# Kernel optimization log

Measured on AMD Instinct MI355X. Metric: run time of the kernel, lower is better.

## Reference

```python
import jax, jax.numpy as jnp
import numpy as np

B, S, D, H, HD, L, E, K, F = 1, 1024, 1024, 16, 64, 64, 8, 2, 4096
EPS = 1e-6


def rms_norm(x):
    return x / jnp.sqrt(jnp.mean(x * x, axis=-1, keepdims=True) + EPS)


def rope_sincos(seq, dim):
    # standard GPT-NeoX-style rotary tables, shape [seq, dim]
    inv = 1.0 / (10000.0 ** (jnp.arange(0, dim, 2, dtype=jnp.float32) / dim))
    ang = jnp.arange(seq, dtype=jnp.float32)[:, None] * inv[None, :]
    sin = jnp.concatenate([jnp.sin(ang), jnp.sin(ang)], axis=-1)
    cos = jnp.concatenate([jnp.cos(ang), jnp.cos(ang)], axis=-1)
    return sin, cos


def apply_rotary(x, sin, cos):
    d = x.shape[-1] // 2
    rot = jnp.concatenate([-x[..., d:], x[..., :d]], axis=-1)
    return x * cos + rot * sin


def setup_inputs() -> dict:
    key = jax.random.key(0)
    ks = jax.random.split(key, 16)
    sd = 0.02

    def nrm(k, shp):
        return jax.random.normal(k, shp, jnp.float32) * sd

    return dict(
        x=jax.random.normal(ks[0], (B, S, D), jnp.float32),
        noise_u=jax.random.uniform(ks[1], (B, S, E), jnp.float32),
        Wdkv=nrm(ks[2], (H, L, HD)),      # per-head w_dkv  (torch weight [L,HD])
        Wq=nrm(ks[3], (H, HD, HD)),       # per-head wq
        Wuv=nrm(ks[4], (H, L, HD)),       # per-head w_uv
        Wuk=nrm(ks[5], (H, L, HD)),       # per-head w_uk
        Wk_rope=nrm(ks[6], (H, L, HD)),   # per-head w_k_rope
        Wq_rope=nrm(ks[7], (H, HD, L)),   # per-head w_q_rope weight
        bq_rope=jnp.zeros((H, HD), jnp.float32),  # w_q_rope bias (Linear default bias=True)
        Wo_head=nrm(ks[8], (H, HD, HD)),  # per-head w_o (no bias)
        Wr=nrm(ks[9], (E, D)),            # router weight
        Wn=nrm(ks[10], (E, D)),           # noise weight
        r_bias=jnp.zeros((E,), jnp.float32),
        W1=nrm(ks[11], (E, D, F)),        # expert fc1 (transposed torch layout)
        b1=jnp.zeros((E, F), jnp.float32),
        W2=nrm(ks[12], (E, F, D)),        # expert fc2
        b2=jnp.zeros((E, D), jnp.float32),
    )


def reference(x, noise_u, Wdkv, Wq, Wuv, Wuk, Wk_rope, Wq_rope, bq_rope,
              Wo_head, Wr, Wn, r_bias, W1, b1, W2, b2):
    # ---- multi-head latent attention (vectorized over heads) ----
    y = rms_norm(x)
    xs = y.reshape(B, S, H, HD).transpose(0, 2, 1, 3)  # [B,H,S,HD]
    sin_k, cos_k = rope_sincos(S, L)
    sin_q, cos_q = rope_sincos(S, HD)

    k = apply_rotary(jnp.einsum('bhsd,hld->bhsl', xs, Wk_rope), sin_k, cos_k)  # [B,H,S,L]
    ckv = jnp.einsum('bhsd,hld->bhsl', xs, Wdkv)                               # [B,H,S,L]
    q = jnp.einsum('bhsl,hdl->bhsd', ckv, Wq_rope) + bq_rope[None, :, None, :]
    q = apply_rotary(q, sin_q, cos_q)                                          # [B,H,S,HD]

    absorbed = jnp.einsum('hqe,hle->hql', Wq, Wuk)                             # [H,HD,L]
    s1 = jnp.einsum('bhsd,hdl,bhtl->bhst', xs, absorbed, ckv)
    s2 = jnp.einsum('bhsd,bhtd->bhst', q, k)
    scores = (s1 + s2) / jnp.sqrt(jnp.float32(2 * HD))
    mask = jnp.tril(jnp.ones((S, S), dtype=bool))  # past_length = 0
    scores = jnp.where(mask, scores, -jnp.inf)
    attn = jax.nn.softmax(scores, axis=-1)

    v = jnp.einsum('bhsl,hld->bhsd', ckv, Wuv)
    o = jnp.einsum('bhst,bhtd->bhsd', attn, v)
    o = jnp.einsum('bhsd,hed->bhse', o, Wo_head)  # per-head w_o (no bias)
    attn_out = o.transpose(0, 2, 1, 3).reshape(B, S, D)
    x = x + attn_out

    # ---- noisy top-k MoE ----
    y2 = rms_norm(x)
    logits = jnp.einsum('bsd,ed->bse', y2, Wr)
    noisy = jnp.einsum('bsd,ed->bse', y2, Wn)
    nl = noise_u * jax.nn.softplus(noisy) + logits + r_bias
    topv, topi = jax.lax.top_k(nl, K)
    gates = jax.nn.softmax(topv, axis=-1)  # softmax over -inf-scattered logits == softmax over top-k
    probs = jnp.sum(gates[..., None] * jax.nn.one_hot(topi, E, dtype=x.dtype), axis=-2)  # [B,S,E]

    h = jax.nn.gelu(jnp.einsum('bsd,edf->ebsf', y2, W1) + b1[:, None, None, :], approximate=False)
    eo = jnp.einsum('ebsf,efd->ebsd', h, W2) + b2[:, None, None, :]
    moe_out = jnp.einsum('bse,ebsd->bsd', probs, eo)
    return x + moe_out
```

## Files before the change

kernel.cpp:

```cpp
#include <hip/hip_runtime.h>
#include <math.h>

#define S_ 1024
#define D_ 1024
#define H_ 16
#define F_ 4096

typedef short s16x8 __attribute__((ext_vector_type(8)));
typedef float fx4 __attribute__((ext_vector_type(4)));

__device__ __forceinline__ float bf2f(unsigned int u){
  union { float f; unsigned int u; } v; v.u = u<<16; return v.f;
}
__device__ __forceinline__ unsigned short f2bf(float f){
  union { float f; unsigned int u; } v; v.f = f;
  unsigned int r = v.u + 0x7fffu + ((v.u>>16)&1u);
  return (unsigned short)(r>>16);
}
__device__ __forceinline__ unsigned int pk2(float a, float b){
  return (unsigned int)f2bf(a) | ((unsigned int)f2bf(b)<<16);
}
__device__ __forceinline__ void gld16(const void* g, void* l){
  typedef const unsigned int __attribute__((address_space(1)))* gp_t;
  typedef unsigned int __attribute__((address_space(3)))* lp_t;
  __builtin_amdgcn_global_load_lds((gp_t)g, (lp_t)l, 16, 0, 0);
}
__device__ __forceinline__ int xcd_swz(int bid, int nwg){
  int q = nwg >> 3;
  return (bid & 7)*q + (bid >> 3);
}

__global__ __launch_bounds__(256) void k_rmsnorm(const float* __restrict__ x, unsigned short* __restrict__ y){
  int row = blockIdx.x, t = threadIdx.x;
  const float4 v = ((const float4*)(x + (size_t)row*D_))[t];
  float ss = v.x*v.x + v.y*v.y + v.z*v.z + v.w*v.w;
  #pragma unroll
  for(int o=1;o<64;o<<=1) ss += __shfl_xor(ss, o);
  __shared__ float red[4];
  if((t&63)==0) red[t>>6]=ss;
  __syncthreads();
  float sc = rsqrtf((red[0]+red[1]+red[2]+red[3])*(1.0f/D_) + 1e-6f);
  ushort4 o4;
  o4.x=f2bf(v.x*sc); o4.y=f2bf(v.y*sc); o4.z=f2bf(v.z*sc); o4.w=f2bf(v.w*sc);
  ((ushort4*)(y + (size_t)row*D_))[t]=o4;
}

__global__ __launch_bounds__(256) void k_prep(const float* __restrict__ Wq,
    const float* __restrict__ Wuk, const float* __restrict__ Wuv,
    float* __restrict__ abs_t, float* __restrict__ wuvt){
  int h = blockIdx.x, tid = threadIdx.x;
  __shared__ float wq[4096], wuk[4096];
  for(int i=tid;i<4096;i+=256){ wq[i]=Wq[h*4096+i]; wuk[i]=Wuk[h*4096+i]; }
  __syncthreads();
  for(int i=tid;i<4096;i+=256){
    float a=0.f;
    #pragma unroll 8
    for(int e=0;e<64;e++) a += wq[(i&63)*64+e]*wuk[(i>>6)*64+e];
    abs_t[h*4096+i]=a;
    wuvt[h*4096+i]=Wuv[h*4096 + (i&63)*64 + (i>>6)];
  }
}

__device__ __forceinline__ void stage_B64(const float* __restrict__ W, unsigned short* Bs, int tid){
  int n = tid>>2, kq = tid&3;
  const float* s = W + n*64 + kq*16;
  float4 f0=*(const float4*)(s), f1=*(const float4*)(s+4), f2=*(const float4*)(s+8), f3=*(const float4*)(s+12);
  ushort4 u0,u1,u2,u3;
  u0.x=f2bf(f0.x);u0.y=f2bf(f0.y);u0.z=f2bf(f0.z);u0.w=f2bf(f0.w);
  u1.x=f2bf(f1.x);u1.y=f2bf(f1.y);u1.z=f2bf(f1.z);u1.w=f2bf(f1.w);
  u2.x=f2bf(f2.x);u2.y=f2bf(f2.y);u2.z=f2bf(f2.z);u2.w=f2bf(f2.w);
  u3.x=f2bf(f3.x);u3.y=f2bf(f3.y);u3.z=f2bf(f3.z);u3.w=f2bf(f3.w);
  int sl0=((kq*2)^(n&7))*8, sl1=((kq*2+1)^(n&7))*8;
  *(ushort4*)&Bs[n*64+sl0]=u0;   *(ushort4*)&Bs[n*64+sl0+4]=u1;
  *(ushort4*)&Bs[n*64+sl1]=u2;   *(ushort4*)&Bs[n*64+sl1+4]=u3;
}
__device__ __forceinline__ void gemm64(const unsigned short* Asrc, const unsigned short* Bs,
    int wv, int l16, int l4, fx4 acc[4]){
  int srow = wv*16 + l16;
  #pragma unroll
  for(int kb=0;kb<2;kb++){
    s16x8 af = *(const s16x8*)&Asrc[srow*64 + (((kb*4+l4)^(srow&7))*8)];
    #pragma unroll
    for(int nf=0;nf<4;nf++){
      int n = nf*16+l16;
      s16x8 bf = *(const s16x8*)&Bs[n*64 + (((kb*4+l4)^(n&7))*8)];
      acc[nf] = __builtin_amdgcn_mfma_f32_16x16x32_bf16(af, bf, acc[nf], 0,0,0);
    }
  }
}

__global__ __launch_bounds__(256) void k_proj_m(const unsigned short* __restrict__ y,
    const float* __restrict__ abs_t, const float* __restrict__ wuvt,
    const float* __restrict__ Wdkv, const float* __restrict__ Wk_rope,
    const float* __restrict__ Wq_rope, const float* __restrict__ bq_rope,
    unsigned short* __restrict__ kk, unsigned short* __restrict__ qq,
    unsigned short* __restrict__ vv){
  __shared__ unsigned short ysd[4096];
  __shared__ unsigned short ckvs[4096];
  __shared__ unsigned short Bs[4096];
  __shared__ unsigned short tmp[64*72];
  const float LNC = 0.28782313662425575f;
  const float ASC = 0.08838834764831845f;
  int s0 = blockIdx.x*64, h = blockIdx.y, tid = threadIdx.x;
  int wv = tid>>6, lane = tid&63, l16 = lane&15, l4 = lane>>4;
  fx4 acc[4];

  {
    int rg = lane>>3, sg = (lane&7)^(rg&7);
    #pragma unroll
    for(int c2=0;c2<2;c2++){
      int c = wv*2+c2;
      gld16(y + (size_t)(s0+c*8+rg)*D_ + h*64 + sg*8, &ysd[c*512]);
    }
  }
  stage_B64(Wdkv + h*4096, Bs, tid);
  __syncthreads();

  #pragma unroll
  for(int nf=0;nf<4;nf++){acc[nf][0]=0.f;acc[nf][1]=0.f;acc[nf][2]=0.f;acc[nf][3]=0.f;}
  gemm64(ysd, Bs, wv, l16, l4, acc);
  #pragma unroll
  for(int nf=0;nf<4;nf++){
    int col = nf*16+l16;
    #pragma unroll
    for(int r=0;r<4;r++){
      int srow = wv*16+4*l4+r;
      ckvs[srow*64 + (((col>>3)^(srow&7))*8) + (col&7)] = f2bf(acc[nf][r]);
    }
  }
  __syncthreads();
  { int row=tid>>2, sl=(tid&3)*2;
    uint4 a=*(const uint4*)&ckvs[row*64+sl*8];
    uint4 b=*(const uint4*)&ckvs[row*64+sl*8+8];
    unsigned short* kr = kk + ((size_t)(h*S_)+s0+row)*128;
    *(uint4*)&kr[(sl^(row&7))*8]=a;
    *(uint4*)&kr[((sl+1)^(row&7))*8]=b;
  }
  stage_B64(Wk_rope + h*4096, Bs, tid);
  __syncthreads();

  #pragma unroll
  for(int nf=0;nf<4;nf++){acc[nf][0]=0.f;acc[nf][1]=0.f;acc[nf][2]=0.f;acc[nf][3]=0.f;}
  gemm64(ysd, Bs, wv, l16, l4, acc);
  #pragma unroll
  for(int nf=0;nf<2;nf++){
    int llo = nf*16+l16;
    float inv = __expf(-(float)llo * LNC);
    #pragma unroll
    for(int r=0;r<4;r++){
      int srow = wv*16+4*l4+r;
      float sn,cs; __sincosf((float)(s0+srow)*inv,&sn,&cs);
      float alo=acc[nf][r], ahi=acc[nf+2][r];
      tmp[srow*72 + llo]      = f2bf(alo*cs - ahi*sn);
      tmp[srow*72 + llo + 32] = f2bf(ahi*cs + alo*sn);
    }
  }
  __syncthreads();
  { int row=tid>>2, c=(tid&3)*16;
    uint4 a=*(const uint4*)&tmp[row*72+c]; uint4 b=*(const uint4*)&tmp[row*72+c+8];
    unsigned short* kr = kk + ((size_t)(h*S_)+s0+row)*128 + 64;
    *(uint4*)&kr[c]=a; *(uint4*)&kr[c+8]=b; }
  stage_B64(Wq_rope + h*4096, Bs, tid);
  __syncthreads();

  #pragma unroll
  for(int nf=0;nf<4;nf++){acc[nf][0]=0.f;acc[nf][1]=0.f;acc[nf][2]=0.f;acc[nf][3]=0.f;}
  gemm64(ckvs, Bs, wv, l16, l4, acc);
  #pragma unroll
  for(int nf=0;nf<4;nf++){
    float bq = bq_rope[h*64 + nf*16+l16];
    #pragma unroll
    for(int r=0;r<4;r++) acc[nf][r]+=bq;
  }
  #pragma unroll
  for(int nf=0;nf<2;nf++){
    int dlo = nf*16+l16;
    float inv = __expf(-(float)dlo * LNC);
    #pragma unroll
    for(int r=0;r<4;r++){
      int srow = wv*16+4*l4+r;
      float sn,cs; __sincosf((float)(s0+srow)*inv,&sn,&cs);
      float alo=acc[nf][r]*ASC, ahi=acc[nf+2][r]*ASC;
      tmp[srow*72 + dlo]      = f2bf(alo*cs - ahi*sn);
      tmp[srow*72 + dlo + 32] = f2bf(ahi*cs + alo*sn);
    }
  }
  __syncthreads();
  { int row=tid>>2, c=(tid&3)*16;
    uint4 a=*(const uint4*)&tmp[row*72+c]; uint4 b=*(const uint4*)&tmp[row*72+c+8];
    unsigned short* qr = qq + ((size_t)(h*S_)+s0+row)*128 + 64;
    *(uint4*)&qr[c]=a; *(uint4*)&qr[c+8]=b; }
  stage_B64(abs_t + h*4096, Bs, tid);
  __syncthreads();

  #pragma unroll
  for(int nf=0;nf<4;nf++){acc[nf][0]=0.f;acc[nf][1]=0.f;acc[nf][2]=0.f;acc[nf][3]=0.f;}
  gemm64(ysd, Bs, wv, l16, l4, acc);
  #pragma unroll
  for(int nf=0;nf<4;nf++)
    #pragma unroll
    for(int r=0;r<4;r++)
      tmp[(wv*16+4*l4+r)*72 + nf*16+l16] = f2bf(acc[nf][r]*ASC);
  __syncthreads();
  { int row=tid>>2, c=(tid&3)*16;
    uint4 a=*(const uint4*)&tmp[row*72+c]; uint4 b=*(const uint4*)&tmp[row*72+c+8];
    unsigned short* qr = qq + ((size_t)(h*S_)+s0+row)*128;
    *(uint4*)&qr[c]=a; *(uint4*)&qr[c+8]=b; }
  stage_B64(wuvt + h*4096, Bs, tid);
  __syncthreads();

  #pragma unroll
  for(int nf=0;nf<4;nf++){acc[nf][0]=0.f;acc[nf][1]=0.f;acc[nf][2]=0.f;acc[nf][3]=0.f;}
  gemm64(ckvs, Bs, wv, l16, l4, acc);
  #pragma unroll
  for(int nf=0;nf<4;nf++)
    #pragma unroll
    for(int r=0;r<4;r++)
      tmp[(wv*16+4*l4+r)*72 + nf*16+l16] = f2bf(acc[nf][r]);
  __syncthreads();
  { int row=tid>>2, c=(tid&3)*16;
    uint4 a=*(const uint4*)&tmp[row*72+c]; uint4 b=*(const uint4*)&tmp[row*72+c+8];
    unsigned short* vr = vv + ((size_t)(h*S_)+s0+row)*64;
    *(uint4*)&vr[c]=a; *(uint4*)&vr[c+8]=b; }
}

__global__ __launch_bounds__(256) void k_attn2(const unsigned short* __restrict__ qq,
    const unsigned short* __restrict__ kk, const unsigned short* __restrict__ vv,
    const float* __restrict__ Wo, const float* __restrict__ x, float* __restrict__ x1){
  __shared__ unsigned short Ks[64*128];
  __shared__ unsigned short Vt[64*72];
  __shared__ unsigned short Pl[4][16*72];
  int h = blockIdx.y, q0 = blockIdx.x*64, tid = threadIdx.x;
  int wave = tid>>6, lane = tid&63;
  int l16 = lane&15, l4 = lane>>4;
  int qglob = q0 + wave*16 + l16;

  s16x8 qf[4];
  {
    const unsigned short* qp = qq + ((size_t)(h*S_)+qglob)*128 + l4*8;
    #pragma unroll
    for(int kb=0;kb<4;kb++) qf[kb] = *(const s16x8*)(qp + kb*32);
  }
  fx4 ot[4];
  #pragma unroll
  for(int t=0;t<4;t++){ ot[t][0]=0.f; ot[t][1]=0.f; ot[t][2]=0.f; ot[t][3]=0.f; }
  float mrun=-1e30f, lrun=0.f;
  int nkt = blockIdx.x + 1;

  for(int kt=0;kt<nkt;kt++){
    int kt0 = kt*64;
    __syncthreads();
    #pragma unroll
    for(int it=0;it<4;it++){
      int idx = tid + it*256;
      int row = idx>>4, c = idx&15;
      uint4 u = *(const uint4*)(kk + ((size_t)(h*S_)+kt0+row)*128 + c*8);
      *(uint4*)&Ks[row*128 + ((c^(row&7))<<3)] = u;
    }
    #pragma unroll
    for(int it=0;it<2;it++){
      int idx = tid + it*256;
      int k = idx>>3, d0 = (idx&7)*8;
      uint4 u = *(const uint4*)(vv + ((size_t)(h*S_)+kt0+k)*64 + d0);
      unsigned short t8[8];
      *(uint4*)t8 = u;
      #pragma unroll
      for(int j=0;j<8;j++) Vt[(d0+j)*72 + k] = t8[j];
    }
    __syncthreads();

    fx4 sa[4];
    #pragma unroll
    for(int i=0;i<4;i++){ sa[i][0]=0.f; sa[i][1]=0.f; sa[i][2]=0.f; sa[i][3]=0.f; }
    #pragma unroll
    for(int kb=0;kb<4;kb++){
      #pragma unroll
      for(int i=0;i<4;i++){
        int row = 16*i + l16;
        s16x8 ak = *(const s16x8*)&Ks[row*128 + (((l4+4*kb)^(row&7))<<3)];
        sa[i] = __builtin_amdgcn_mfma_f32_16x16x32_bf16(ak, qf[kb], sa[i], 0,0,0);
      }
    }
    float pv[16]; float mloc=-1e30f;
    #pragma unroll
    for(int i=0;i<4;i++)
      #pragma unroll
      for(int r=0;r<4;r++){
        int kg = kt0 + 16*i + 4*l4 + r;
        float s = (kg<=qglob)? sa[i][r] : -1e30f;
        pv[i*4+r]=s; mloc=fmaxf(mloc,s);
      }
    mloc = fmaxf(mloc, __shfl_xor(mloc,16));
    mloc = fmaxf(mloc, __shfl_xor(mloc,32));
    float mnew = fmaxf(mrun,mloc);
    float alpha = __expf(mrun-mnew);
    float psum=0.f;
    #pragma unroll
    for(int z=0;z<16;z++){ pv[z]=__expf(pv[z]-mnew); psum+=pv[z]; }
    psum += __shfl_xor(psum,16); psum += __shfl_xor(psum,32);
    lrun = lrun*alpha + psum; mrun = mnew;
    #pragma unroll
    for(int t=0;t<4;t++){ ot[t][0]*=alpha; ot[t][1]*=alpha; ot[t][2]*=alpha; ot[t][3]*=alpha; }
    {
      unsigned short* pw = &Pl[wave][l16*72 + 4*l4];
      #pragma unroll
      for(int i=0;i<4;i++){
        *(unsigned int*)&pw[16*i]   = pk2(pv[i*4+0],pv[i*4+1]);
        *(unsigned int*)&pw[16*i+2] = pk2(pv[i*4+2],pv[i*4+3]);
      }
    }
    #pragma unroll
    for(int kb=0;kb<2;kb++){
      s16x8 pf = *(const s16x8*)&Pl[wave][l16*72 + kb*32 + l4*8];
      #pragma unroll
      for(int t=0;t<4;t++){
        s16x8 av = *(const s16x8*)&Vt[(16*t+l16)*72 + kb*32 + l4*8];
        ot[t] = __builtin_amdgcn_mfma_f32_16x16x32_bf16(av, pf, ot[t], 0,0,0);
      }
    }
  }

  float invl = 1.f/lrun;
  {
    unsigned short* pw = &Pl[wave][l16*72 + 4*l4];
    #pragma unroll
    for(int t=0;t<4;t++){
      *(unsigned int*)&pw[16*t]   = pk2(ot[t][0]*invl, ot[t][1]*invl);
      *(unsigned int*)&pw[16*t+2] = pk2(ot[t][2]*invl, ot[t][3]*invl);
    }
  }
  __syncthreads();
  #pragma unroll
  for(int it=0;it<4;it++){
    int idx = tid + it*256;
    int ee = idx>>4, dd = (idx&15)*4;
    float4 wv = *(const float4*)(Wo + h*4096 + ee*64 + dd);
    ushort4 w4; w4.x=f2bf(wv.x); w4.y=f2bf(wv.y); w4.z=f2bf(wv.z); w4.w=f2bf(wv.w);
    *(ushort4*)&Vt[ee*72 + dd] = w4;
  }
  __syncthreads();
  fx4 outT[4];
  #pragma unroll
  for(int t=0;t<4;t++){ outT[t][0]=0.f; outT[t][1]=0.f; outT[t][2]=0.f; outT[t][3]=0.f; }
  #pragma unroll
  for(int kb=0;kb<2;kb++){
    s16x8 of = *(const s16x8*)&Pl[wave][l16*72 + kb*32 + l4*8];
    #pragma unroll
    for(int t=0;t<4;t++){
      s16x8 aw = *(const s16x8*)&Vt[(16*t+l16)*72 + kb*32 + l4*8];
      outT[t] = __builtin_amdgcn_mfma_f32_16x16x32_bf16(aw, of, outT[t], 0,0,0);
    }
  }
  #pragma unroll
  for(int t=0;t<4;t++){
    size_t base = (size_t)qglob*D_ + h*64 + 16*t + 4*l4;
    float4 xv = *(const float4*)(x + base);
    float4 r;
    r.x = xv.x + outT[t][0]; r.y = xv.y + outT[t][1];
    r.z = xv.z + outT[t][2]; r.w = xv.w + outT[t][3];
    *(float4*)(x1+base) = r;
  }
}

__global__ __launch_bounds__(64) void k_gate(const float* __restrict__ x1, const float* __restrict__ Wr,
    const float* __restrict__ Wn, const float* __restrict__ r_bias, const float* __restrict__ noise_u,
    float* __restrict__ gates, int* __restrict__ topi, unsigned short* __restrict__ y2){
  int s = blockIdx.x, lane = threadIdx.x;
  const float* xr = x1 + (size_t)s*D_ + lane*16;
  float yv[16]; float ss=0.f;
  #pragma unroll
  for(int i=0;i<16;i+=4){
    float4 a = *(const float4*)(xr+i);
    yv[i]=a.x; yv[i+1]=a.y; yv[i+2]=a.z; yv[i+3]=a.w;
    ss += a.x*a.x+a.y*a.y+a.z*a.z+a.w*a.w;
  }
  #pragma unroll
  for(int o=1;o<64;o<<=1) ss += __shfl_xor(ss,o);
  float sc = rsqrtf(ss*(1.0f/D_) + 1e-6f);
  #pragma unroll
  for(int i=0;i<16;i++) yv[i]*=sc;
  {
    unsigned short* yo = y2 + (size_t)s*D_ + lane*16;
    ushort4 o0,o1,o2,o3;
    o0.x=f2bf(yv[0]); o0.y=f2bf(yv[1]); o0.z=f2bf(yv[2]); o0.w=f2bf(yv[3]);
    o1.x=f2bf(yv[4]); o1.y=f2bf(yv[5]); o1.z=f2bf(yv[6]); o1.w=f2bf(yv[7]);
    o2.x=f2bf(yv[8]); o2.y=f2bf(yv[9]); o2.z=f2bf(yv[10]); o2.w=f2bf(yv[11]);
    o3.x=f2bf(yv[12]); o3.y=f2bf(yv[13]); o3.z=f2bf(yv[14]); o3.w=f2bf(yv[15]);
    *(ushort4*)(yo)   = o0; *(ushort4*)(yo+4) = o1;
    *(ushort4*)(yo+8) = o2; *(ushort4*)(yo+12)= o3;
  }
  float lg[8], nz[8];
  #pragma unroll
  for(int e=0;e<8;e++){
    const float* wr = Wr + e*D_ + lane*16;
    const float* wn = Wn + e*D_ + lane*16;
    float a=0.f,b=0.f;
    #pragma unroll
    for(int i=0;i<16;i+=4){
      float4 w1 = *(const float4*)(wr+i); float4 w2 = *(const float4*)(wn+i);
      a += yv[i]*w1.x + yv[i+1]*w1.y + yv[i+2]*w1.z + yv[i+3]*w1.w;
      b += yv[i]*w2.x + yv[i+1]*w2.y + yv[i+2]*w2.z + yv[i+3]*w2.w;
    }
    lg[e]=a; nz[e]=b;
  }
  #pragma unroll
  for(int o=1;o<64;o<<=1){
    #pragma unroll
    for(int e=0;e<8;e++){ lg[e]+=__shfl_xor(lg[e],o); nz[e]+=__shfl_xor(nz[e],o); }
  }
  if(lane==0){
    float nl[8];
    for(int e=0;e<8;e++){
      float z = nz[e];
      float sp = (z>20.f)? z : log1pf(expf(z));
      nl[e] = noise_u[s*8+e]*sp + lg[e] + r_bias[e];
    }
    int i0=0; float v0=nl[0];
    for(int e=1;e<8;e++) if(nl[e]>v0){v0=nl[e];i0=e;}
    float v1=-1e30f; int i1=0;
    for(int e=0;e<8;e++) if(e!=i0 && nl[e]>v1){v1=nl[e];i1=e;}
    float ex = expf(v1-v0);
    gates[s*2]   = 1.f/(1.f+ex);
    gates[s*2+1] = ex/(1.f+ex);
    topi[s*2]=i0; topi[s*2+1]=i1;
  }
}

__global__ __launch_bounds__(256) void k_lists(const int* __restrict__ topi,
    int* __restrict__ offs, int* __restrict__ pair_tok, int* __restrict__ slot_of){
  __shared__ int tp[2048];
  __shared__ int cnt[8];
  __shared__ int off_s[9];
  int t = threadIdx.x;
  int wave = t>>6, lane = t&63;
  unsigned long long below = (lane==63)? 0xFFFFFFFFFFFFFFFFull>>1
                                       : ((1ull<<lane)-1ull);
  for(int i=t;i<2048;i+=256) tp[i]=topi[i];
  __syncthreads();
  #pragma unroll
  for(int sub=0;sub<2;sub++){
    int e = wave*2+sub;
    int c=0;
    for(int ch=0;ch<32;ch++) c += (tp[ch*64+lane]==e);
    #pragma unroll
    for(int o=1;o<64;o<<=1) c += __shfl_xor(c,o);
    if(lane==0) cnt[e]=c;
  }
  __syncthreads();
  if(t==0){
    int a=0;
    for(int e=0;e<8;e++){ off_s[e]=a; a += (cnt[e]+127)&~127; }
    off_s[8]=a;
    for(int e=0;e<9;e++) offs[e]=off_s[e];
  }
  __syncthreads();
  #pragma unroll
  for(int sub=0;sub<2;sub++){
    int e = wave*2+sub;
    int base = off_s[e];
    for(int ch=0;ch<32;ch++){
      int idx = ch*64+lane;
      bool pred = (tp[idx]==e);
      unsigned long long mask = __ballot(pred);
      if(pred){
        int slot = base + __popcll(mask & below);
        pair_tok[slot] = idx>>1;
        slot_of[idx] = slot;
      }
      base += __popcll(mask);
    }
    for(int slot=base+lane; slot<off_s[e+1]; slot+=64) pair_tok[slot]=0;
  }
}

__global__ __launch_bounds__(256) void k_cvt_t(const float* __restrict__ src,
    unsigned short* __restrict__ dst, int R, int C){
  __shared__ float ts[64][65];
  int e = blockIdx.z;
  int r0 = blockIdx.x*64, c0 = blockIdx.y*64;
  const float* s = src + (size_t)e*R*C;
  unsigned short* d = dst + (size_t)e*R*C;
  int t = threadIdx.x;
  #pragma unroll
  for(int it=0; it<4; it++){
    int flat = it*256+t;
    int r = flat>>4, cq = (flat&15)*4;
    float4 v = *(const float4*)(s + (size_t)(r0+r)*C + c0+cq);
    ts[r][cq]=v.x; ts[r][cq+1]=v.y; ts[r][cq+2]=v.z; ts[r][cq+3]=v.w;
  }
  __syncthreads();
  #pragma unroll
  for(int it=0; it<4; it++){
    int flat = it*256+t;
    int c = flat>>4, kq = (flat&15)*4;
    ushort4 o;
    o.x=f2bf(ts[kq][c]); o.y=f2bf(ts[kq+1][c]); o.z=f2bf(ts[kq+2][c]); o.w=f2bf(ts[kq+3][c]);
    *(ushort4*)(d + (size_t)(c0+c)*R + r0+kq) = o;
  }
}

__global__ __launch_bounds__(256) void k_fc1t(const unsigned short* __restrict__ y2,
    const int* __restrict__ pair_tok, const int* __restrict__ offs,
    const unsigned short* __restrict__ Bt, const float* __restrict__ bias1,
    unsigned short* __restrict__ hbuf){
  __shared__ unsigned short As[2][8192];
  __shared__ unsigned short Bs[2][8192];
  __shared__ int sh_e;
  int tid=threadIdx.x, lane=tid&63, wv=tid>>6;
  int swz = xcd_swz(blockIdx.x, 768);
  int r0 = (swz % 24)*128, n0 = (swz / 24)*128;
  if(tid==0){ int e=-1; if(r0<offs[8]){e=0; while(offs[e+1]<=r0) e++;} sh_e=e; }
  __syncthreads();
  int e=sh_e; if(e<0) return;
  int rg = lane>>3;
  int sg = (lane&7)^(rg&7);
  const unsigned short* aptr[4];
  const unsigned short* bptr[4];
  #pragma unroll
  for(int c=0;c<4;c++){
    int ch = wv*4+c;
    int tok = pair_tok[r0 + ch*8 + rg];
    aptr[c] = y2 + (size_t)tok*D_ + sg*8;
    bptr[c] = Bt + (size_t)e*D_*F_ + (size_t)(n0 + ch*8 + rg)*D_ + sg*8;
  }
  int l16=lane&15, l4=lane>>4;
  int wm=wv>>1, wn=wv&1;
  fx4 acc[4][4];
  #pragma unroll
  for(int a0=0;a0<4;a0++)
    #pragma unroll
    for(int b0=0;b0<4;b0++){ acc[a0][b0][0]=0.f; acc[a0][b0][1]=0.f; acc[a0][b0][2]=0.f; acc[a0][b0][3]=0.f; }

  #pragma unroll
  for(int c=0;c<4;c++){
    gld16(aptr[c], &As[0][(wv*4+c)*512]);
    gld16(bptr[c], &Bs[0][(wv*4+c)*512]);
  }

  int buf=0;
  for(int kt=0;kt<D_;kt+=64){
    asm volatile("s_waitcnt vmcnt(0)" ::: "memory");
    asm volatile("s_barrier" ::: "memory");
    s16x8 af[2][4], bf[2][4];
    #pragma unroll
    for(int kb=0;kb<2;kb++){
      #pragma unroll
      for(int mf=0;mf<4;mf++){
        int row = wm*64+mf*16+l16;
        af[kb][mf] = *(const s16x8*)&As[buf][row*64 + (((kb*4+l4)^(row&7))*8)];
      }
      #pragma unroll
      for(int nf=0;nf<4;nf++){
        int col = wn*64+nf*16+l16;
        bf[kb][nf] = *(const s16x8*)&Bs[buf][col*64 + (((kb*4+l4)^(col&7))*8)];
      }
    }
    if(kt+64<D_){
      #pragma unroll
      for(int c=0;c<4;c++){
        gld16(aptr[c]+kt+64, &As[buf^1][(wv*4+c)*512]);
        gld16(bptr[c]+kt+64, &Bs[buf^1][(wv*4+c)*512]);
      }
    }
    __builtin_amdgcn_sched_barrier(0);
    __builtin_amdgcn_s_setprio(1);
    #pragma unroll
    for(int kb=0;kb<2;kb++)
      #pragma unroll
      for(int mf=0;mf<4;mf++)
        #pragma unroll
        for(int nf=0;nf<4;nf++)
          acc[mf][nf]=__builtin_amdgcn_mfma_f32_16x16x32_bf16(af[kb][mf],bf[kb][nf],acc[mf][nf],0,0,0);
    __builtin_amdgcn_s_setprio(0);
    asm volatile("s_barrier" ::: "memory");
    buf ^= 1;
  }
  #pragma unroll
  for(int mf=0;mf<4;mf++)
    #pragma unroll
    for(int nf=0;nf<4;nf++){
      int gcol=n0+wn*64+nf*16+l16;
      float bias=bias1[e*F_+gcol];
      #pragma unroll
      for(int rgi=0;rgi<4;rgi++){
        int grow=r0+wm*64+mf*16+l4*4+rgi;
        float vv=acc[mf][nf][rgi]+bias;
        float g=0.5f*vv*(1.f+erff(vv*0.70710678118654752f));
        hbuf[(size_t)grow*F_+gcol]=f2bf(g);
      }
    }
}

__global__ __launch_bounds__(256) void k_fc2t(const unsigned short* __restrict__ hbuf,
    const int* __restrict__ offs, const unsigned short* __restrict__ Bt,
    const float* __restrict__ bias2, float* __restrict__ eo, int klen, int parts){
  __shared__ unsigned short As[2][8192];
  __shared__ unsigned short Bs[2][4096];
  __shared__ int sh_e;
  int tid=threadIdx.x, lane=tid&63, wv=tid>>6;
  int nwg = 384*parts;
  int swz = xcd_swz(blockIdx.x, nwg);
  int kz  = swz / 384;
  int rem = swz % 384;
  int r0 = (rem % 24)*128, n0 = (rem / 24)*64;
  int k0 = kz*klen;
  if(tid==0){ int e=-1; if(r0<offs[8]){e=0; while(offs[e+1]<=r0) e++;} sh_e=e; }
  __syncthreads();
  int e=sh_e; if(e<0) return;
  int rg = lane>>3;
  int sg = (lane&7)^(rg&7);
  const unsigned short* aptr[4];
  const unsigned short* bptr[2];
  #pragma unroll
  for(int c=0;c<4;c++){
    int ch = wv*4+c;
    aptr[c] = hbuf + (size_t)(r0 + ch*8 + rg)*F_ + k0 + sg*8;
  }
  #pragma unroll
  for(int c=0;c<2;c++){
    int ch = wv*2+c;
    bptr[c] = Bt + (size_t)e*F_*D_ + (size_t)(n0 + ch*8 + rg)*F_ + k0 + sg*8;
  }
  int l16=lane&15, l4=lane>>4;
  fx4 acc[2][4];
  #pragma unroll
  for(int a0=0;a0<2;a0++)
    #pragma unroll
    for(int b0=0;b0<4;b0++){ acc[a0][b0][0]=0.f; acc[a0][b0][1]=0.f; acc[a0][b0][2]=0.f; acc[a0][b0][3]=0.f; }

  #pragma unroll
  for(int c=0;c<4;c++) gld16(aptr[c], &As[0][(wv*4+c)*512]);
  #pragma unroll
  for(int c=0;c<2;c++) gld16(bptr[c], &Bs[0][(wv*2+c)*512]);

  int buf=0;
  for(int kt=0;kt<klen;kt+=64){
    asm volatile("s_waitcnt vmcnt(0)" ::: "memory");
    asm volatile("s_barrier" ::: "memory");
    s16x8 af[2][2], bf[2][4];
    #pragma unroll
    for(int kb=0;kb<2;kb++){
      #pragma unroll
      for(int mf=0;mf<2;mf++){
        int row = wv*32+mf*16+l16;
        af[kb][mf] = *(const s16x8*)&As[buf][row*64 + (((kb*4+l4)^(row&7))*8)];
      }
      #pragma unroll
      for(int nf=0;nf<4;nf++){
        int col = nf*16+l16;
        bf[kb][nf] = *(const s16x8*)&Bs[buf][col*64 + (((kb*4+l4)^(col&7))*8)];
      }
    }
    if(kt+64<klen){
      #pragma unroll
      for(int c=0;c<4;c++) gld16(aptr[c]+kt+64, &As[buf^1][(wv*4+c)*512]);
      #pragma unroll
      for(int c=0;c<2;c++) gld16(bptr[c]+kt+64, &Bs[buf^1][(wv*2+c)*512]);
    }
    __builtin_amdgcn_sched_barrier(0);
    __builtin_amdgcn_s_setprio(1);
    #pragma unroll
    for(int kb=0;kb<2;kb++)
      #pragma unroll
      for(int mf=0;mf<2;mf++)
        #pragma unroll
        for(int nf=0;nf<4;nf++)
          acc[mf][nf]=__builtin_amdgcn_mfma_f32_16x16x32_bf16(af[kb][mf],bf[kb][nf],acc[mf][nf],0,0,0);
    __builtin_amdgcn_s_setprio(0);
    asm volatile("s_barrier" ::: "memory");
    buf ^= 1;
  }
  float* eop = eo + (size_t)kz*3072*D_;
  #pragma unroll
  for(int mf=0;mf<2;mf++)
    #pragma unroll
    for(int nf=0;nf<4;nf++){
      int gcol=n0+nf*16+l16;
      float bias=(kz==0)? bias2[e*D_+gcol] : 0.f;
      #pragma unroll
      for(int rgi=0;rgi<4;rgi++){
        int grow=r0+wv*32+mf*16+l4*4+rgi;
        eop[(size_t)grow*D_+gcol]=acc[mf][nf][rgi]+bias;
      }
    }
}

__global__ __launch_bounds__(256) void k_fc1_fb(const unsigned short* __restrict__ y2,
    const int* __restrict__ pair_tok, const int* __restrict__ offs,
    const float* __restrict__ W1, const float* __restrict__ bias1,
    unsigned short* __restrict__ hbuf){
  __shared__ unsigned short As[4096];
  __shared__ unsigned short Bs[4096];
  __shared__ int sh_e;
  int tid=threadIdx.x;
  int r0=blockIdx.x*128, n0=blockIdx.y*128;
  if(tid==0){ int e=-1; if(r0<offs[8]){ e=0; while(offs[e+1]<=r0) e++; } sh_e=e; }
  __syncthreads();
  int e=sh_e; if(e<0) return;
  const float* Bsrc = W1 + (size_t)e*D_*F_;
  int r=tid&127, hf=tid>>7;
  int tok=pair_tok[r0+r];
  const unsigned short* Asrc = y2 + (size_t)tok*D_ + hf*16;
  int pk=tid>>5, pn=tid&31;
  int lane=tid&63, wvid=tid>>6;
  int wm=wvid>>1, wn=wvid&1;
  int l16=lane&15, l4=lane>>4;
  fx4 acc[4][4];
  #pragma unroll
  for(int a0=0;a0<4;a0++)
    #pragma unroll
    for(int b0=0;b0<4;b0++){ acc[a0][b0][0]=0.f; acc[a0][b0][1]=0.f; acc[a0][b0][2]=0.f; acc[a0][b0][3]=0.f; }
  for(int kt=0;kt<D_;kt+=32){
    uint4 av0=*(const uint4*)(Asrc+kt);
    uint4 av1=*(const uint4*)(Asrc+kt+8);
    const float* bp=Bsrc+(size_t)(kt+pk*4)*F_+n0+pn*4;
    float4 bv0=*(const float4*)(bp);
    float4 bv1=*(const float4*)(bp+F_);
    float4 bv2=*(const float4*)(bp+2*F_);
    float4 bv3=*(const float4*)(bp+3*F_);
    *(uint4*)&As[(hf*2)*1024 + r*8]=av0;
    *(uint4*)&As[(hf*2+1)*1024 + r*8]=av1;
    unsigned short c0[4]={f2bf(bv0.x),f2bf(bv0.y),f2bf(bv0.z),f2bf(bv0.w)};
    unsigned short c1[4]={f2bf(bv1.x),f2bf(bv1.y),f2bf(bv1.z),f2bf(bv1.w)};
    unsigned short c2[4]={f2bf(bv2.x),f2bf(bv2.y),f2bf(bv2.z),f2bf(bv2.w)};
    unsigned short c3[4]={f2bf(bv3.x),f2bf(bv3.y),f2bf(bv3.z),f2bf(bv3.w)};
    #pragma unroll
    for(int j2=0;j2<4;j2++){
      int col=pn*4+j2;
      int kb=(pk*4)^(((col>>2)&3)<<3);
      ushort4 wr;
      wr.x=c0[j2]; wr.y=c1[j2]; wr.z=c2[j2]; wr.w=c3[j2];
      *(ushort4*)&Bs[col*32+kb]=wr;
    }
    __syncthreads();
    s16x8 af[4],bf8[4];
    #pragma unroll
    for(int mf=0;mf<4;mf++){
      int rowl=wm*64+mf*16+l16;
      af[mf]=*(const s16x8*)&As[l4*1024+rowl*8];
    }
    #pragma unroll
    for(int nf=0;nf<4;nf++){
      int col=wn*64+nf*16+l16;
      int kb=(l4*8)^(((col>>2)&3)<<3);
      bf8[nf]=*(const s16x8*)&Bs[col*32+kb];
    }
    #pragma unroll
    for(int mf=0;mf<4;mf++)
      #pragma unroll
      for(int nf=0;nf<4;nf++)
        acc[mf][nf]=__builtin_amdgcn_mfma_f32_16x16x32_bf16(af[mf],bf8[nf],acc[mf][nf],0,0,0);
    __syncthreads();
  }
  #pragma unroll
  for(int mf=0;mf<4;mf++)
    #pragma unroll
    for(int nf=0;nf<4;nf++){
      int gcol=n0+wn*64+nf*16+l16;
      float bias=bias1[e*F_+gcol];
      #pragma unroll
      for(int rg=0;rg<4;rg++){
        int grow=r0+wm*64+mf*16+l4*4+rg;
        float vv=acc[mf][nf][rg]+bias;
        float g=0.5f*vv*(1.f+erff(vv*0.70710678118654752f));
        hbuf[(size_t)grow*F_+gcol]=f2bf(g);
      }
    }
}

__global__ __launch_bounds__(256) void k_fc2_fb(const unsigned short* __restrict__ hbuf,
    const int* __restrict__ offs, const float* __restrict__ W2,
    const float* __restrict__ bias2, float* __restrict__ eo){
  __shared__ unsigned short As[4096];
  __shared__ unsigned short Bs[2048];
  __shared__ int sh_e;
  int tid=threadIdx.x;
  int r0=blockIdx.x*128, n0=blockIdx.y*64;
  if(tid==0){ int e=-1; if(r0<offs[8]){ e=0; while(offs[e+1]<=r0) e++; } sh_e=e; }
  __syncthreads();
  int e=sh_e; if(e<0) return;
  const float* Bsrc=W2+(size_t)e*F_*D_;
  int r=tid&127, hf=tid>>7;
  const unsigned short* Asrc=hbuf+(size_t)(r0+r)*F_+hf*16;
  int pk=tid>>4, pn=tid&15;
  int lane=tid&63, wvid=tid>>6;
  int l16=lane&15, l4=lane>>4;
  fx4 acc[2][4];
  #pragma unroll
  for(int a0=0;a0<2;a0++)
    #pragma unroll
    for(int b0=0;b0<4;b0++){ acc[a0][b0][0]=0.f; acc[a0][b0][1]=0.f; acc[a0][b0][2]=0.f; acc[a0][b0][3]=0.f; }
  for(int kt=0;kt<F_;kt+=32){
    uint4 av0=*(const uint4*)(Asrc+kt);
    uint4 av1=*(const uint4*)(Asrc+kt+8);
    const float* bp=Bsrc+(size_t)(kt+pk*2)*D_+n0+pn*4;
    float4 bv0=*(const float4*)bp;
    float4 bv1=*(const float4*)(bp+D_);
    *(uint4*)&As[(hf*2)*1024+r*8]=av0;
    *(uint4*)&As[(hf*2+1)*1024+r*8]=av1;
    unsigned short c0[4]={f2bf(bv0.x),f2bf(bv0.y),f2bf(bv0.z),f2bf(bv0.w)};
    unsigned short c1[4]={f2bf(bv1.x),f2bf(bv1.y),f2bf(bv1.z),f2bf(bv1.w)};
    #pragma unroll
    for(int j2=0;j2<4;j2++){
      int col=pn*4+j2;
      int kb=(pk*2)^(((col>>2)&3)<<3);
      unsigned int pack=(unsigned int)c0[j2] | ((unsigned int)c1[j2]<<16);
      *(unsigned int*)&Bs[col*32+kb]=pack;
    }
    __syncthreads();
    s16x8 af[2],bf8[4];
    #pragma unroll
    for(int mf=0;mf<2;mf++){
      int rowl=wvid*32+mf*16+l16;
      af[mf]=*(const s16x8*)&As[l4*1024+rowl*8];
    }
    #pragma unroll
    for(int nf=0;nf<4;nf++){
      int col=nf*16+l16;
      int kb=(l4*8)^(((col>>2)&3)<<3);
      bf8[nf]=*(const s16x8*)&Bs[col*32+kb];
    }
    #pragma unroll
    for(int mf=0;mf<2;mf++)
      #pragma unroll
      for(int nf=0;nf<4;nf++)
        acc[mf][nf]=__builtin_amdgcn_mfma_f32_16x16x32_bf16(af[mf],bf8[nf],acc[mf][nf],0,0,0);
    __syncthreads();
  }
  #pragma unroll
  for(int mf=0;mf<2;mf++)
    #pragma unroll
    for(int nf=0;nf<4;nf++){
      int gcol=n0+nf*16+l16;
      float bias=bias2[e*D_+gcol];
      #pragma unroll
      for(int rg=0;rg<4;rg++){
        int grow=r0+wvid*32+mf*16+l4*4+rg;
        eo[(size_t)grow*D_+gcol]=acc[mf][nf][rg]+bias;
      }
    }
}

__global__ __launch_bounds__(256) void k_combine(const float* __restrict__ x1, const float* __restrict__ eo,
    int parts, const float* __restrict__ gates, const int* __restrict__ slot_of, float* __restrict__ out){
  int s=blockIdx.x, t=threadIdx.x;
  float g0=gates[s*2], g1=gates[s*2+1];
  int a0=slot_of[s*2], a1=slot_of[s*2+1];
  float4 o=((const float4*)(x1+(size_t)s*D_))[t];
  for(int p=0;p<parts;p++){
    const float* ep = eo + (size_t)p*3072*D_;
    float4 e0=((const float4*)(ep+(size_t)a0*D_))[t];
    float4 e1=((const float4*)(ep+(size_t)a1*D_))[t];
    o.x+=g0*e0.x+g1*e1.x;
    o.y+=g0*e0.y+g1*e1.y;
    o.z+=g0*e0.z+g1*e1.z;
    o.w+=g0*e0.w+g1*e1.w;
  }
  ((float4*)(out+(size_t)s*D_))[t]=o;
}

extern "C" void kernel_launch(void* const* d_in, const int* in_sizes, int n_in,
                              void* d_out, int out_size, void* d_ws, size_t ws_size,
                              hipStream_t stream){
  (void)in_sizes; (void)n_in; (void)out_size;
  const float* x       = (const float*)d_in[0];
  const float* noise_u = (const float*)d_in[1];
  const float* Wdkv    = (const float*)d_in[2];
  const float* Wq      = (const float*)d_in[3];
  const float* Wuv     = (const float*)d_in[4];
  const float* Wuk     = (const float*)d_in[5];
  const float* Wk_rope = (const float*)d_in[6];
  const float* Wq_rope = (const float*)d_in[7];
  const float* bq_rope = (const float*)d_in[8];
  const float* Wo_head = (const float*)d_in[9];
  const float* Wr      = (const float*)d_in[10];
  const float* Wn      = (const float*)d_in[11];
  const float* r_bias  = (const float*)d_in[12];
  const float* W1      = (const float*)d_in[13];
  const float* b1      = (const float*)d_in[14];
  const float* W2      = (const float*)d_in[15];
  const float* b2      = (const float*)d_in[16];
  float* out           = (float*)d_out;

  char* w = (char*)d_ws;
  unsigned short* y    = (unsigned short*)(w);
  unsigned short* kk   = (unsigned short*)(w + 2097152);
  unsigned short* qq   = (unsigned short*)(w + 6291456);
  unsigned short* vv   = (unsigned short*)(w + 10485760);
  float* abs_t         = (float*)(w + 12582912);
  float* wuvt          = (float*)(w + 12845056);
  float* x1            = (float*)(w + 13107200);
  unsigned short* y2   = (unsigned short*)(w + 17301504);
  float* gates         = (float*)(w + 19398656);
  int* topi            = (int*)(w + 19406848);
  int* slot_of         = (int*)(w + 19415040);
  int* offs            = (int*)(w + 19423232);
  int* pair_tok        = (int*)(w + 19427328);
  unsigned short* hbuf = (unsigned short*)(w + 19443712);
  float* eo            = (float*)(w + 44609536);

  const size_t NEED4 = 162050048ull;
  const size_t NEED2 = 136884224ull;
  int parts; unsigned short* Wt;
  if(ws_size >= NEED4){ parts = 4; Wt = (unsigned short*)(w + 94941184); }
  else if(ws_size >= NEED2){ parts = 2; Wt = (unsigned short*)(w + 69775360); }
  else { parts = 0; Wt = 0; }

  if(parts){
    k_cvt_t<<<dim3(16,64,8),256,0,stream>>>(W1, Wt, D_, F_);
  }
  k_rmsnorm<<<S_,256,0,stream>>>(x, y);
  k_prep<<<H_,256,0,stream>>>(Wq, Wuk, Wuv, abs_t, wuvt);
  k_proj_m<<<dim3(16,H_),256,0,stream>>>(y, abs_t, wuvt, Wdkv, Wk_rope, Wq_rope, bq_rope, kk, qq, vv);
  k_attn2<<<dim3(16,H_),256,0,stream>>>(qq, kk, vv, Wo_head, x, x1);
  k_gate<<<S_,64,0,stream>>>(x1, Wr, Wn, r_bias, noise_u, gates, topi, y2);
  k_lists<<<1,256,0,stream>>>(topi, offs, pair_tok, slot_of);
  if(parts){
    k_fc1t<<<768,256,0,stream>>>(y2, pair_tok, offs, Wt, b1, hbuf);
    k_cvt_t<<<dim3(64,16,8),256,0,stream>>>(W2, Wt, F_, D_);
    k_fc2t<<<384*parts,256,0,stream>>>(hbuf, offs, Wt, b2, eo, F_/parts, parts);
    k_combine<<<S_,256,0,stream>>>(x1, eo, parts, gates, slot_of, out);
  } else {
    k_fc1_fb<<<dim3(24,32),256,0,stream>>>(y2, pair_tok, offs, W1, b1, hbuf);
    k_fc2_fb<<<dim3(24,16),256,0,stream>>>(hbuf, offs, W2, b2, eo);
    k_combine<<<S_,256,0,stream>>>(x1, eo, 1, gates, slot_of, out);
  }
}
```

Baseline: 288.9 us.

## Enlarge expert FC1 tile to 256x256 with 512 threads and pad experts to 256

The expert FC1 GEMM moves from 128x128 tiles on 256 threads to 256x256 tiles on 512 threads (8 waves, each covering 128x64). The K-step is split into two half-steps so only one half's fragments are held in registers at a time. Per-expert row padding rises from 128 to 256 to match the new tile, and the FC2 grid, eo stride and workspace offsets grow to fit up to 4096 padded rows. The aim is more operand reuse per LDS load and fewer global reads of W1. In exchange it adds wasted padded rows in both FC1 and FC2, launches fewer FC1 blocks than the GPU has CUs, and uses about 128KB of LDS per block.

Measured after the change: 400.7 us. 1.39x slower.

```diff
diff --git a/kernel.cpp b/kernel.cpp
--- a/kernel.cpp
+++ b/kernel.cpp
@@ -449,7 +449,7 @@
   __syncthreads();
   if(t==0){
     int a=0;
-    for(int e=0;e<8;e++){ off_s[e]=a; a += (cnt[e]+127)&~127; }
+    for(int e=0;e<8;e++){ off_s[e]=a; a += (cnt[e]+255)&~255; }
     off_s[8]=a;
     for(int e=0;e<9;e++) offs[e]=off_s[e];
   }
@@ -499,16 +499,16 @@
   }
 }
 
-__global__ __launch_bounds__(256) void k_fc1t(const unsigned short* __restrict__ y2,
+__global__ __launch_bounds__(512) void k_fc1t(const unsigned short* __restrict__ y2,
     const int* __restrict__ pair_tok, const int* __restrict__ offs,
     const unsigned short* __restrict__ Bt, const float* __restrict__ bias1,
     unsigned short* __restrict__ hbuf){
-  __shared__ unsigned short As[2][8192];
-  __shared__ unsigned short Bs[2][8192];
+  __shared__ unsigned short As[2][16384];
+  __shared__ unsigned short Bs[2][16384];
   __shared__ int sh_e;
   int tid=threadIdx.x, lane=tid&63, wv=tid>>6;
-  int swz = xcd_swz(blockIdx.x, 768);
-  int r0 = (swz % 24)*128, n0 = (swz / 24)*128;
+  int swz = xcd_swz(blockIdx.x, 256);
+  int r0 = (swz & 15)*256, n0 = (swz >> 4)*256;
   if(tid==0){ int e=-1; if(r0<offs[8]){e=0; while(offs[e+1]<=r0) e++;} sh_e=e; }
   __syncthreads();
   int e=sh_e; if(e<0) return;
@@ -524,10 +524,10 @@
     bptr[c] = Bt + (size_t)e*D_*F_ + (size_t)(n0 + ch*8 + rg)*D_ + sg*8;
   }
   int l16=lane&15, l4=lane>>4;
-  int wm=wv>>1, wn=wv&1;
-  fx4 acc[4][4];
-  #pragma unroll
-  for(int a0=0;a0<4;a0++)
+  int wm=wv>>2, wn=wv&3;
+  fx4 acc[8][4];
+  #pragma unroll
+  for(int a0=0;a0<8;a0++)
     #pragma unroll
     for(int b0=0;b0<4;b0++){ acc[a0][b0][0]=0.f; acc[a0][b0][1]=0.f; acc[a0][b0][2]=0.f; acc[a0][b0][3]=0.f; }
 
@@ -541,49 +541,66 @@
   for(int kt=0;kt<D_;kt+=64){
     asm volatile("s_waitcnt vmcnt(0)" ::: "memory");
     asm volatile("s_barrier" ::: "memory");
-    s16x8 af[2][4], bf[2][4];
-    #pragma unroll
-    for(int kb=0;kb<2;kb++){
-      #pragma unroll
-      for(int mf=0;mf<4;mf++){
-        int row = wm*64+mf*16+l16;
-        af[kb][mf] = *(const s16x8*)&As[buf][row*64 + (((kb*4+l4)^(row&7))*8)];
+    {
+      s16x8 af[8], bf[4];
+      #pragma unroll
+      for(int mf=0;mf<8;mf++){
+        int row = wm*128+mf*16+l16;
+        af[mf] = *(const s16x8*)&As[buf][row*64 + ((l4^(row&7))*8)];
       }
       #pragma unroll
       for(int nf=0;nf<4;nf++){
         int col = wn*64+nf*16+l16;
-        bf[kb][nf] = *(const s16x8*)&Bs[buf][col*64 + (((kb*4+l4)^(col&7))*8)];
-      }
-    }
-    if(kt+64<D_){
-      #pragma unroll
-      for(int c=0;c<4;c++){
-        gld16(aptr[c]+kt+64, &As[buf^1][(wv*4+c)*512]);
-        gld16(bptr[c]+kt+64, &Bs[buf^1][(wv*4+c)*512]);
-      }
-    }
-    __builtin_amdgcn_sched_barrier(0);
-    __builtin_amdgcn_s_setprio(1);
-    #pragma unroll
-    for(int kb=0;kb<2;kb++)
-      #pragma unroll
-      for(int mf=0;mf<4;mf++)
+        bf[nf] = *(const s16x8*)&Bs[buf][col*64 + ((l4^(col&7))*8)];
+      }
+      __builtin_amdgcn_s_setprio(1);
+      #pragma unroll
+      for(int mf=0;mf<8;mf++)
         #pragma unroll
         for(int nf=0;nf<4;nf++)
-          acc[mf][nf]=__builtin_amdgcn_mfma_f32_16x16x32_bf16(af[kb][mf],bf[kb][nf],acc[mf][nf],0,0,0);
-    __builtin_amdgcn_s_setprio(0);
+          acc[mf][nf]=__builtin_amdgcn_mfma_f32_16x16x32_bf16(af[mf],bf[nf],acc[mf][nf],0,0,0);
+      __builtin_amdgcn_s_setprio(0);
+    }
+    {
+      s16x8 af[8], bf[4];
+      #pragma unroll
+      for(int mf=0;mf<8;mf++){
+        int row = wm*128+mf*16+l16;
+        af[mf] = *(const s16x8*)&As[buf][row*64 + (((4+l4)^(row&7))*8)];
+      }
+      #pragma unroll
+      for(int nf=0;nf<4;nf++){
+        int col = wn*64+nf*16+l16;
+        bf[nf] = *(const s16x8*)&Bs[buf][col*64 + (((4+l4)^(col&7))*8)];
+      }
+      if(kt+64<D_){
+        #pragma unroll
+        for(int c=0;c<4;c++){
+          gld16(aptr[c]+kt+64, &As[buf^1][(wv*4+c)*512]);
+          gld16(bptr[c]+kt+64, &Bs[buf^1][(wv*4+c)*512]);
+        }
+      }
+      __builtin_amdgcn_sched_barrier(0);
+      __builtin_amdgcn_s_setprio(1);
+      #pragma unroll
+      for(int mf=0;mf<8;mf++)
+        #pragma unroll
+        for(int nf=0;nf<4;nf++)
+          acc[mf][nf]=__builtin_amdgcn_mfma_f32_16x16x32_bf16(af[mf],bf[nf],acc[mf][nf],0,0,0);
+      __builtin_amdgcn_s_setprio(0);
+    }
     asm volatile("s_barrier" ::: "memory");
     buf ^= 1;
   }
   #pragma unroll
-  for(int mf=0;mf<4;mf++)
+  for(int mf=0;mf<8;mf++)
     #pragma unroll
     for(int nf=0;nf<4;nf++){
       int gcol=n0+wn*64+nf*16+l16;
       float bias=bias1[e*F_+gcol];
       #pragma unroll
       for(int rgi=0;rgi<4;rgi++){
-        int grow=r0+wm*64+mf*16+l4*4+rgi;
+        int grow=r0+wm*128+mf*16+l4*4+rgi;
         float vv=acc[mf][nf][rgi]+bias;
         float g=0.5f*vv*(1.f+erff(vv*0.70710678118654752f));
         hbuf[(size_t)grow*F_+gcol]=f2bf(g);
@@ -598,11 +615,11 @@
   __shared__ unsigned short Bs[2][4096];
   __shared__ int sh_e;
   int tid=threadIdx.x, lane=tid&63, wv=tid>>6;
-  int nwg = 384*parts;
+  int nwg = 512*parts;
   int swz = xcd_swz(blockIdx.x, nwg);
-  int kz  = swz / 384;
-  int rem = swz % 384;
-  int r0 = (rem % 24)*128, n0 = (rem / 24)*64;
+  int kz  = swz / 512;
+  int rem = swz % 512;
+  int r0 = (rem & 31)*128, n0 = (rem >> 5)*64;
   int k0 = kz*klen;
   if(tid==0){ int e=-1; if(r0<offs[8]){e=0; while(offs[e+1]<=r0) e++;} sh_e=e; }
   __syncthreads();
@@ -670,7 +687,7 @@
     asm volatile("s_barrier" ::: "memory");
     buf ^= 1;
   }
-  float* eop = eo + (size_t)kz*3072*D_;
+  float* eop = eo + (size_t)kz*4096*D_;
   #pragma unroll
   for(int mf=0;mf<2;mf++)
     #pragma unroll
@@ -848,7 +865,7 @@
   int a0=slot_of[s*2], a1=slot_of[s*2+1];
   float4 o=((const float4*)(x1+(size_t)s*D_))[t];
   for(int p=0;p<parts;p++){
-    const float* ep = eo + (size_t)p*3072*D_;
+    const float* ep = eo + (size_t)p*4096*D_;
     float4 e0=((const float4*)(ep+(size_t)a0*D_))[t];
     float4 e1=((const float4*)(ep+(size_t)a1*D_))[t];
     o.x+=g0*e0.x+g1*e1.x;
@@ -897,13 +914,13 @@
   int* offs            = (int*)(w + 19423232);
   int* pair_tok        = (int*)(w + 19427328);
   unsigned short* hbuf = (unsigned short*)(w + 19443712);
-  float* eo            = (float*)(w + 44609536);
-
-  const size_t NEED4 = 162050048ull;
-  const size_t NEED2 = 136884224ull;
+  float* eo            = (float*)(w + 52998144);
+
+  const size_t NEED4 = 187215872ull;
+  const size_t NEED2 = 153661440ull;
   int parts; unsigned short* Wt;
-  if(ws_size >= NEED4){ parts = 4; Wt = (unsigned short*)(w + 94941184); }
-  else if(ws_size >= NEED2){ parts = 2; Wt = (unsigned short*)(w + 69775360); }
+  if(ws_size >= NEED4){ parts = 4; Wt = (unsigned short*)(w + 120107008); }
+  else if(ws_size >= NEED2){ parts = 2; Wt = (unsigned short*)(w + 86552576); }
   else { parts = 0; Wt = 0; }
 
   if(parts){
@@ -916,13 +933,13 @@
   k_gate<<<S_,64,0,stream>>>(x1, Wr, Wn, r_bias, noise_u, gates, topi, y2);
   k_lists<<<1,256,0,stream>>>(topi, offs, pair_tok, slot_of);
   if(parts){
-    k_fc1t<<<768,256,0,stream>>>(y2, pair_tok, offs, Wt, b1, hbuf);
+    k_fc1t<<<256,512,0,stream>>>(y2, pair_tok, offs, Wt, b1, hbuf);
     k_cvt_t<<<dim3(64,16,8),256,0,stream>>>(W2, Wt, F_, D_);
-    k_fc2t<<<384*parts,256,0,stream>>>(hbuf, offs, Wt, b2, eo, F_/parts, parts);
+    k_fc2t<<<512*parts,256,0,stream>>>(hbuf, offs, Wt, b2, eo, F_/parts, parts);
     k_combine<<<S_,256,0,stream>>>(x1, eo, parts, gates, slot_of, out);
   } else {
-    k_fc1_fb<<<dim3(24,32),256,0,stream>>>(y2, pair_tok, offs, W1, b1, hbuf);
-    k_fc2_fb<<<dim3(24,16),256,0,stream>>>(hbuf, offs, W2, b2, eo);
+    k_fc1_fb<<<dim3(32,32),256,0,stream>>>(y2, pair_tok, offs, W1, b1, hbuf);
+    k_fc2_fb<<<dim3(32,16),256,0,stream>>>(hbuf, offs, W2, b2, eo);
     k_combine<<<S_,256,0,stream>>>(x1, eo, 1, gates, slot_of, out);
   }
 }
```
